# Kernel tuning notes

Measured on AMD Instinct MI355X. Metric: run time of the kernel, lower is better.

The kernel has to match this reference:

```python
import jax, jax.numpy as jnp
import numpy as np

N_ATOMS = 65536
N_PAIRS = N_ATOMS * 32
MAXZ = 95          # D3 tables cover H..Pu, indexed directly by atomic number
NREF = 5           # number of reference coordination numbers per element
CUTOFF, CUTON = 12.0, 10.0   # model units; distances_model2Bohr == 1
K1, K3 = 16.0, -4.0
SMALL = 1e-30      # fp32 stand-in for the original's 1e-300 double guard


def setup_inputs() -> dict:
    key = jax.random.key(0)
    k0, k1, k2, k3 = jax.random.split(key, 4)
    rng = np.random.default_rng(0)

    atomic_numbers = jax.random.randint(k0, (N_ATOMS,), 1, 87)
    idx_i = jax.random.randint(k1, (N_PAIRS,), 0, N_ATOMS)
    idx_j = jax.random.randint(k2, (N_PAIRS,), 0, N_ATOMS)
    # pair distances spanning inside/switch/outside of the 10..12 cutoff band
    distances = jax.random.uniform(k3, (N_PAIRS,), minval=0.8, maxval=12.5)

    # synthetic stand-ins for the grimme_d3 data files
    rcov = jnp.asarray(rng.uniform(0.5, 3.0, (MAXZ,)).astype(np.float32))
    rcn_np = rng.uniform(0.0, 5.0, (MAXZ, NREF)).astype(np.float32)
    rcn_np[::3, NREF - 1] = -1.0  # mimic -1 padding for missing references
    rcn = jnp.asarray(rcn_np)
    rc6 = jnp.asarray(rng.uniform(1.0, 50.0, (MAXZ, MAXZ, NREF, NREF)).astype(np.float32))
    r2r4 = jnp.asarray(rng.uniform(1.0, 10.0, (MAXZ,)).astype(np.float32))

    s6 = jnp.float32(1.0)
    s8 = jnp.float32(0.9171)
    a1 = jnp.float32(0.3385)
    a2 = jnp.float32(2.883)
    return dict(distances=distances, rcov=rcov, rcn=rcn, rc6=rc6, r2r4=r2r4,
                s6=s6, s8=s8, a1=a1, a2=a2,
                atomic_numbers=atomic_numbers, idx_i=idx_i, idx_j=idx_j)


def reference(distances, rcov, rcn, rc6, r2r4, s6, s8, a1, a2,
              atomic_numbers, idx_i, idx_j):
    n = atomic_numbers.shape[0]
    zi = atomic_numbers[idx_i]
    zj = atomic_numbers[idx_j]

    # smooth switch-off from 1 (r < cuton) to 0 (r >= cutoff)
    x = (CUTOFF - distances) / (CUTOFF - CUTON)
    sw = jnp.where(distances < CUTON, 1.0,
                   jnp.where(distances >= CUTOFF, 0.0,
                             ((6.0 * x - 15.0) * x + 10.0) * x * x * x))

    # coordination numbers via inverse damping, scatter-summed per atom i
    rcov_ij = rcov[zi] + rcov[zj]
    cn_ij = sw / (1.0 + jnp.exp(-K1 * (rcov_ij / distances - 1.0)))
    cn = jax.ops.segment_sum(cn_ij, idx_i, num_segments=n)  # [N]

    # Gaussian weights over reference CNs (soft retrieval into rc6 table)
    rcn_a = rcn[atomic_numbers]                 # [N, NREF]
    mask = rcn_a >= 0
    dcn = rcn_a - cn[:, None]
    gw = jnp.where(mask, jnp.exp(K3 * dcn * dcn), 0.0)
    norm = jnp.sum(gw, axis=-1, keepdims=True)
    # exceptional case: all gaussians underflow -> pick the max reference CN
    rcn_max_a = jnp.max(rcn, axis=-1)[atomic_numbers][:, None]
    exceptional = (rcn_a == rcn_max_a).astype(gw.dtype)
    weights = jnp.where(norm == 0, exceptional, gw / jnp.maximum(norm, SMALL))  # [N, NREF]

    # weighted pairwise C6 from reference table rc6[Zi, Zj, a, b]
    w_i = weights[idx_i]                         # [P, NREF]
    w_j = weights[idx_j]                         # [P, NREF]
    c6 = jnp.einsum('pa,pb,pab->p', w_i, w_j, rc6[zi, zj])

    # C8 = 3 * C6 * <r2>/<r4>_i * <r2>/<r4>_j ; BJ critical radius
    qq = 3.0 * r2r4[zi] * r2r4[zj]
    rr = a1 * jnp.sqrt(qq) + a2

    d2 = distances * distances
    d6 = d2 * d2 * d2
    d8 = d6 * d2
    rr2 = rr * rr
    rr6 = rr2 * rr2 * rr2
    rr8 = rr6 * rr2

    # BJ-damped dispersion energy per pair (0.5 for double counting), switched
    e_pair = -0.5 * (s6 * c6 / (d6 + rr6) + s8 * qq * c6 / (d8 + rr8)) * sw

    # per-atom dispersion energies (energies_Hartree2model == 1)
    return jax.ops.segment_sum(e_pair, idx_i, num_segments=n)
```

## Files before the change

### kernel.cpp

```cpp
#include <hip/hip_runtime.h>
#include <stdint.h>


typedef unsigned short u16;
#define MAXZ 95
#define NREF 5
#define EXC_CUT -87.33654f
#define NB    1024
#define BSH   6
#define BSZ   64
#define CAPSH 12
#define SBLOCKS 256
#define TILE  16384
#define RC_TOTAL (MAXZ * MAXZ * 32)

__device__ __forceinline__ float h2f(u16 h) {
    union { _Float16 h; u16 u; } v; v.u = h; return (float)v.h;
}
__device__ __forceinline__ u16 f2h(float f) {
    union { _Float16 h; u16 u; } v; v.h = (_Float16)f; return v.u;
}

__device__ __forceinline__ float switch_fn(float d) {
    if (d < 10.0f) return 1.0f;
    float x = (12.0f - d) * 0.5f;
    return ((6.0f * x - 15.0f) * x + 10.0f) * x * x * x;
}

__device__ __forceinline__ void calc_weights(const float* __restrict__ rcn_z,
                                             float cni, float* __restrict__ w) {
    float r[NREF], arg[NREF];
    float rmax = -1e30f, marg = -1e30f;
#pragma unroll
    for (int a = 0; a < NREF; a++) {
        r[a] = rcn_z[a];
        rmax = fmaxf(rmax, r[a]);
        float dc = r[a] - cni;
        arg[a] = (-4.0f * dc) * dc;
        if (r[a] >= 0.0f) marg = fmaxf(marg, arg[a]);
    }
    if (marg < EXC_CUT) {
#pragma unroll
        for (int a = 0; a < NREF; a++) w[a] = (r[a] == rmax) ? 1.0f : 0.0f;
    } else {
        float g[NREF], norm = 0.0f;
#pragma unroll
        for (int a = 0; a < NREF; a++) {
            float e = (r[a] >= 0.0f) ? expf(arg[a]) : 0.0f;
            g[a] = e;
            norm += e;
        }
        float inv = 1.0f / fmaxf(norm, 1e-30f);
#pragma unroll
        for (int a = 0; a < NREF; a++) w[a] = g[a] * inv;
    }
}

__global__ __launch_bounds__(1024) void scatter_pairs(const float* __restrict__ dist,
                                                      const int* __restrict__ idx_i,
                                                      const int* __restrict__ idx_j,
                                                      const int* __restrict__ Z,
                                                      const float* __restrict__ rcov,
                                                      const float* __restrict__ rc6,
                                                      float* __restrict__ rcovA,
                                                      u16* __restrict__ rc6pad,
                                                      uint32_t* __restrict__ bcount,
                                                      uint2* __restrict__ recs,
                                                      int n_pairs, int n_atoms,
                                                      int chunk) {
    __shared__ uint2 stage[TILE];
    __shared__ uint32_t hist[NB];
    __shared__ uint32_t startb[NB];
    __shared__ uint32_t cur[NB];
    __shared__ uint32_t res[NB];
    __shared__ uint32_t wsum[16];

    int tid = (int)threadIdx.x;
    int g = blockIdx.x * 1024 + tid;
    int T = gridDim.x * 1024;
    for (int i = g; i < n_atoms; i += T) rcovA[i] = rcov[Z[i]];
    for (int id = g; id < RC_TOTAL; id += T) {
        int tile = id >> 5, slot = id & 31;
        rc6pad[id] = (slot < 25) ? f2h(rc6[(size_t)tile * 25 + slot]) : (u16)0;
    }

    int lo = blockIdx.x * chunk;
    int hi = min(lo + chunk, n_pairs);

    for (int t0 = lo; t0 < hi; t0 += TILE) {
        int tend = min(t0 + TILE, hi);
        hist[tid] = 0;
        __syncthreads();

        uint32_t rx[16], ry[16], vm = 0;
#pragma unroll
        for (int it = 0; it < 4; it++) {
            int q0 = t0 + tid * 4 + it * 4096;
            int m = (q0 < tend) ? min(4, tend - q0) : 0;
            float d4[4]; int i4[4], j4[4];
            if (m == 4) {
                float4 dv = *(const float4*)(dist + q0);
                int4 iv = *(const int4*)(idx_i + q0);
                int4 jv = *(const int4*)(idx_j + q0);
                d4[0] = dv.x; d4[1] = dv.y; d4[2] = dv.z; d4[3] = dv.w;
                i4[0] = iv.x; i4[1] = iv.y; i4[2] = iv.z; i4[3] = iv.w;
                j4[0] = jv.x; j4[1] = jv.y; j4[2] = jv.z; j4[3] = jv.w;
            } else {
                for (int s = 0; s < m; s++) {
                    d4[s] = dist[q0 + s]; i4[s] = idx_i[q0 + s]; j4[s] = idx_j[q0 + s];
                }
            }
#pragma unroll
            for (int s = 0; s < 4; s++) {
                int k = it * 4 + s;
                rx[k] = 0u; ry[k] = 0u;
                if (s < m && d4[s] < 12.0f) {
                    uint32_t i = (uint32_t)i4[s];
                    uint32_t b = i >> BSH;
                    rx[k] = __float_as_uint(d4[s]);
                    ry[k] = ((uint32_t)j4[s] & 0xFFFFu) |
                            ((i & (BSZ - 1u)) << 16) | (b << 22);
                    vm |= (1u << k);
                    atomicAdd(&hist[b], 1u);
                }
            }
        }
        __syncthreads();

        {
            uint32_t h = hist[tid];
            int lane = tid & 63, w = tid >> 6;
            uint32_t inc = h;
#pragma unroll
            for (int off = 1; off < 64; off <<= 1) {
                uint32_t v = __shfl_up(inc, off, 64);
                if (lane >= off) inc += v;
            }
            if (lane == 63) wsum[w] = inc;
            __syncthreads();
            if (tid < 16) {
                uint32_t v = wsum[tid];
                uint32_t s = v;
#pragma unroll
                for (int off = 1; off < 16; off <<= 1) {
                    uint32_t u = __shfl_up(s, off, 64);
                    if (tid >= off) s += u;
                }
                wsum[tid] = s - v;
            }
            __syncthreads();
            uint32_t sb = (inc - h) + wsum[w];
            startb[tid] = sb;
            cur[tid] = sb;
            res[tid] = h ? atomicAdd(&bcount[tid], h) : 0u;
        }
        __syncthreads();

#pragma unroll
        for (int k = 0; k < 16; k++) {
            if (vm & (1u << k)) {
                uint32_t b = ry[k] >> 22;
                uint32_t pos = atomicAdd(&cur[b], 1u);
                stage[pos] = make_uint2(rx[k], ry[k]);
            }
        }
        __syncthreads();

        uint32_t total = startb[NB - 1] + hist[NB - 1];
        for (uint32_t t = (uint32_t)tid; t < total; t += 1024u) {
            uint2 r = stage[t];
            uint32_t b = r.y >> 22;
            uint32_t gpos = res[b] + (t - startb[b]);
            if (gpos < (1u << CAPSH))
                recs[((size_t)b << CAPSH) + gpos] =
                    make_uint2(r.x, r.y & 0x3FFFFFu);
        }
        __syncthreads();
    }
}

__global__ __launch_bounds__(256) void cn_weights_bucket(const uint2* __restrict__ recs,
                                                         const uint32_t* __restrict__ bcount,
                                                         const float* __restrict__ rcovA,
                                                         const int* __restrict__ Z,
                                                         const float* __restrict__ rcn,
                                                         const float* __restrict__ r2r4,
                                                         uint4* __restrict__ arec_h,
                                                         int n_atoms) {
    __shared__ float lrc[BSZ];
    __shared__ float acc[BSZ];
    int b = blockIdx.x;
    int base = b << BSH;
    if (threadIdx.x < BSZ) {
        int i = base + (int)threadIdx.x;
        lrc[threadIdx.x] = (i < n_atoms) ? rcovA[i] : 0.0f;
        acc[threadIdx.x] = 0.0f;
    }
    __syncthreads();
    uint32_t n = min(bcount[b], 1u << CAPSH);
    const uint2* r0 = recs + ((size_t)b << CAPSH);
    if (n) {
        uint32_t nm1 = n - 1;
        uint32_t k = threadIdx.x;
        uint2 recA = r0[min(k, nm1)];
        uint2 recB = r0[min(k + 256, nm1)];
        float rjA = rcovA[recA.y & 0xFFFF];
        for (; k < n; k += 256) {
            uint2 recC = r0[min(k + 512, nm1)];
            float rjB = rcovA[recB.y & 0xFFFF];
            float d = __uint_as_float(recA.x);
            int il = (recA.y >> 16) & (BSZ - 1);
            float rij = lrc[il] + rjA;
            float sw = switch_fn(d);
            atomicAdd(&acc[il], sw / (1.0f + expf(-16.0f * (rij / d - 1.0f))));
            recA = recB; recB = recC; rjA = rjB;
        }
    }
    __syncthreads();
    if (threadIdx.x < BSZ) {
        int i = base + (int)threadIdx.x;
        if (i < n_atoms) {
            int z = Z[i];
            float w[NREF];
            calc_weights(rcn + (size_t)z * NREF, acc[threadIdx.x], w);
            uint4 pk;
            pk.x = (uint32_t)f2h(w[0]) | ((uint32_t)f2h(w[1]) << 16);
            pk.y = (uint32_t)f2h(w[2]) | ((uint32_t)f2h(w[3]) << 16);
            pk.z = (uint32_t)f2h(w[4]) | ((uint32_t)f2h(r2r4[z]) << 16);
            pk.w = (uint32_t)z;
            arec_h[i] = pk;
        }
    }
}

__global__ __launch_bounds__(256) void energy_bucket(const uint2* __restrict__ recs,
                                                     const uint32_t* __restrict__ bcount,
                                                     const uint4* __restrict__ arec_h,
                                                     const u16* __restrict__ rc6pad,
                                                     const float* __restrict__ s6p,
                                                     const float* __restrict__ s8p,
                                                     const float* __restrict__ a1p,
                                                     const float* __restrict__ a2p,
                                                     float* __restrict__ eout,
                                                     int n_atoms) {
    __shared__ float4 la0[BSZ];
    __shared__ float4 la1[BSZ];
    __shared__ float  acc[BSZ];
    int b = blockIdx.x;
    int base = b << BSH;
    if (threadIdx.x < BSZ) {
        int i = min(base + (int)threadIdx.x, n_atoms - 1);
        uint4 pk = arec_h[i];
        la0[threadIdx.x] = make_float4(h2f(pk.x & 0xFFFFu), h2f(pk.x >> 16),
                                       h2f(pk.y & 0xFFFFu), h2f(pk.y >> 16));
        la1[threadIdx.x] = make_float4(h2f(pk.z & 0xFFFFu), h2f(pk.z >> 16),
                                       __int_as_float((int)pk.w), 0.0f);
        acc[threadIdx.x] = 0.0f;
    }
    __syncthreads();
    float s6 = s6p[0], s8 = s8p[0], a1 = a1p[0], a2 = a2p[0];
    uint32_t n = min(bcount[b], 1u << CAPSH);
    const uint2* r0 = recs + ((size_t)b << CAPSH);
    if (n) {
        uint32_t nm1 = n - 1;
        uint32_t k = threadIdx.x;
        uint2 recA = r0[min(k, nm1)];
        uint2 recB = r0[min(k + 256, nm1)];
        uint4 pjA = arec_h[recA.y & 0xFFFFu];
        for (; k < n; k += 256) {
            uint2 recC = r0[min(k + 512, nm1)];
            uint4 pjB = arec_h[recB.y & 0xFFFFu];

            int il = (recA.y >> 16) & (BSZ - 1);
            float4 ai1 = la1[il];
            int zi = __float_as_int(ai1.z);
            int zj = (int)pjA.w;
            const uint4* T4 = (const uint4*)(rc6pad + (size_t)(zi * MAXZ + zj) * 32);
            uint4 t0 = T4[0], t1 = T4[1], t2 = T4[2];
            uint32_t t3 = ((const uint32_t*)T4)[12];

            float d = __uint_as_float(recA.x);
            float4 ai0 = la0[il];
            float wi[NREF] = {ai0.x, ai0.y, ai0.z, ai0.w, ai1.x};
            float wj[NREF] = {h2f(pjA.x & 0xFFFFu), h2f(pjA.x >> 16),
                              h2f(pjA.y & 0xFFFFu), h2f(pjA.y >> 16),
                              h2f(pjA.z & 0xFFFFu)};
            float r2r4j = h2f(pjA.z >> 16);

            float tt[25];
            uint32_t tw[12] = {t0.x, t0.y, t0.z, t0.w, t1.x, t1.y, t1.z, t1.w,
                               t2.x, t2.y, t2.z, t2.w};
#pragma unroll
            for (int k2 = 0; k2 < 12; k2++) {
                tt[2 * k2]     = h2f((u16)(tw[k2] & 0xFFFFu));
                tt[2 * k2 + 1] = h2f((u16)(tw[k2] >> 16));
            }
            tt[24] = h2f((u16)(t3 & 0xFFFFu));

            float c6 = 0.0f;
#pragma unroll
            for (int a = 0; a < NREF; a++) {
                float ss = 0.0f;
#pragma unroll
                for (int bb = 0; bb < NREF; bb++) ss = fmaf(wj[bb], tt[a * NREF + bb], ss);
                c6 = fmaf(wi[a], ss, c6);
            }

            float qq = 3.0f * ai1.y * r2r4j;
            float rr = a1 * sqrtf(qq) + a2;
            float d2 = d * d;
            float d6 = d2 * d2 * d2;
            float d8 = d6 * d2;
            float rr2 = rr * rr;
            float rr6 = rr2 * rr2 * rr2;
            float rr8 = rr6 * rr2;
            float sw = switch_fn(d);

            float e = -0.5f * (s6 * c6 / (d6 + rr6) + s8 * qq * c6 / (d8 + rr8)) * sw;
            atomicAdd(&acc[il], e);

            recA = recB; recB = recC; pjA = pjB;
        }
    }
    __syncthreads();
    if (threadIdx.x < BSZ) {
        int i = base + (int)threadIdx.x;
        if (i < n_atoms) eout[i] = acc[threadIdx.x];
    }
}

__global__ __launch_bounds__(256) void pair_cn_slim(const float* __restrict__ dist,
                                                    const float* __restrict__ rcov,
                                                    const int* __restrict__ Z,
                                                    const int* __restrict__ idx_i,
                                                    const int* __restrict__ idx_j,
                                                    float* __restrict__ cn,
                                                    int n_pairs) {
    int p = blockIdx.x * blockDim.x + threadIdx.x;
    if (p >= n_pairs) return;
    float d = dist[p];
    if (d >= 12.0f) return;
    float rij = rcov[Z[idx_i[p]]] + rcov[Z[idx_j[p]]];
    float sw = switch_fn(d);
    atomicAdd(&cn[idx_i[p]], sw / (1.0f + expf(-16.0f * (rij / d - 1.0f))));
}

__global__ __launch_bounds__(256) void pair_energy_slim(const float* __restrict__ dist,
                                                        const int* __restrict__ Z,
                                                        const int* __restrict__ idx_i,
                                                        const int* __restrict__ idx_j,
                                                        const float* __restrict__ cn,
                                                        const float* __restrict__ rcn,
                                                        const float* __restrict__ r2r4,
                                                        const float* __restrict__ rc6,
                                                        const float* __restrict__ s6p,
                                                        const float* __restrict__ s8p,
                                                        const float* __restrict__ a1p,
                                                        const float* __restrict__ a2p,
                                                        float* __restrict__ eout,
                                                        int n_pairs) {
    int p = blockIdx.x * blockDim.x + threadIdx.x;
    if (p >= n_pairs) return;
    float d = dist[p];
    if (d >= 12.0f) return;
    int i = idx_i[p], j = idx_j[p];
    int zi = Z[i], zj = Z[j];
    float wi[NREF], wj[NREF];
    calc_weights(rcn + (size_t)zi * NREF, cn[i], wi);
    calc_weights(rcn + (size_t)zj * NREF, cn[j], wj);
    const float* T = rc6 + (size_t)(zi * MAXZ + zj) * 25;
    float c6 = 0.0f;
#pragma unroll
    for (int a = 0; a < NREF; a++) {
        float s = 0.0f;
#pragma unroll
        for (int bb = 0; bb < NREF; bb++) s = fmaf(wj[bb], T[a * NREF + bb], s);
        c6 = fmaf(wi[a], s, c6);
    }
    float qq = 3.0f * r2r4[zi] * r2r4[zj];
    float rr = a1p[0] * sqrtf(qq) + a2p[0];
    float d2 = d * d;
    float d6 = d2 * d2 * d2;
    float d8 = d6 * d2;
    float rr2 = rr * rr;
    float rr6 = rr2 * rr2 * rr2;
    float rr8 = rr6 * rr2;
    float sw = switch_fn(d);
    float e = -0.5f * (s6p[0] * c6 / (d6 + rr6) + s8p[0] * qq * c6 / (d8 + rr8)) * sw;
    atomicAdd(&eout[i], e);
}

extern "C" void kernel_launch(void* const* d_in, const int* in_sizes, int n_in,
                              void* d_out, int out_size, void* d_ws, size_t ws_size,
                              hipStream_t stream) {
    const float* dist = (const float*)d_in[0];
    const float* rcov = (const float*)d_in[1];
    const float* rcn  = (const float*)d_in[2];
    const float* rc6  = (const float*)d_in[3];
    const float* r2r4 = (const float*)d_in[4];
    const float* s6p  = (const float*)d_in[5];
    const float* s8p  = (const float*)d_in[6];
    const float* a1p  = (const float*)d_in[7];
    const float* a2p  = (const float*)d_in[8];
    const int* Z    = (const int*)d_in[9];
    const int* idxi = (const int*)d_in[10];
    const int* idxj = (const int*)d_in[11];
    float* out = (float*)d_out;

    int n_pairs = in_sizes[0];
    int n_atoms = in_sizes[9];

    char* ws = (char*)d_ws;
    size_t o_bcount = 0;
    size_t o_rcovA  = 4096;
    size_t o_arec   = (o_rcovA + (size_t)n_atoms * 4 + 15) & ~(size_t)15;
    size_t o_rc6    = (o_arec + (size_t)n_atoms * 16 + 63) & ~(size_t)63;
    size_t o_recs   = (o_rc6 + (size_t)RC_TOTAL * 2 + 255) & ~(size_t)255;
    size_t need     = o_recs + ((size_t)NB << CAPSH) * 8;

    uint32_t* bcount = (uint32_t*)(ws + o_bcount);
    float* rcovA  = (float*)(ws + o_rcovA);
    uint4* arec_h = (uint4*)(ws + o_arec);
    u16*   rcpad  = (u16*)(ws + o_rc6);
    uint2* recs   = (uint2*)(ws + o_recs);

    if (ws_size >= need && n_atoms <= NB * BSZ && n_atoms <= 65536) {
        hipMemsetAsync(bcount, 0, NB * 4, stream);
        int chunk = (n_pairs + SBLOCKS - 1) / SBLOCKS;
        scatter_pairs<<<SBLOCKS, 1024, 0, stream>>>(dist, idxi, idxj, Z, rcov, rc6,
                                                    rcovA, rcpad, bcount, recs,
                                                    n_pairs, n_atoms, chunk);
        cn_weights_bucket<<<NB, 256, 0, stream>>>(recs, bcount, rcovA, Z, rcn, r2r4,
                                                  arec_h, n_atoms);
        energy_bucket<<<NB, 256, 0, stream>>>(recs, bcount, arec_h, rcpad,
                                              s6p, s8p, a1p, a2p, out, n_atoms);
    } else {
        int pgrid = (n_pairs + 255) / 256;
        float* cn = (float*)(ws + o_rcovA);
        hipMemsetAsync(out, 0, (size_t)n_atoms * 4, stream);
        hipMemsetAsync(cn, 0, (size_t)n_atoms * 4, stream);
        pair_cn_slim<<<pgrid, 256, 0, stream>>>(dist, rcov, Z, idxi, idxj, cn, n_pairs);
        pair_energy_slim<<<pgrid, 256, 0, stream>>>(dist, Z, idxi, idxj, cn, rcn, r2r4,
                                                    rc6, s6p, s8p, a1p, a2p, out, n_pairs);
    }
}
```

Before: 139.3 us.

## Fuse CN-weights and energy passes into one cooperative kernel with grid sync

Merges the coordination-number/weights kernel and the energy kernel into one cooperative launch, separated by a grid-wide barrier. The goal is to save one kernel launch and its inter-kernel gap. If the cooperative launch fails, it falls back to the two separate kernels. It also halves the number of scatter blocks from 256 to 128. In exchange, the grid sync costs time, and 1024 co-resident blocks of 256 threads are needed, which may limit occupancy or make the cooperative launch fail.

```diff
diff --git a/kernel.cpp b/kernel.cpp
--- a/kernel.cpp
+++ b/kernel.cpp
@@ -1,6 +1,9 @@
 #include <hip/hip_runtime.h>
+#include <hip/hip_cooperative_groups.h>
 #include <stdint.h>
 
+
+namespace cg = cooperative_groups;
 
 typedef unsigned short u16;
 #define MAXZ 95
@@ -10,7 +13,7 @@
 #define BSH   6
 #define BSZ   64
 #define CAPSH 12
-#define SBLOCKS 256
+#define SBLOCKS 128
 #define TILE  16384
 #define RC_TOTAL (MAXZ * MAXZ * 32)
 
@@ -179,16 +182,17 @@
     }
 }
 
-__global__ __launch_bounds__(256) void cn_weights_bucket(const uint2* __restrict__ recs,
-                                                         const uint32_t* __restrict__ bcount,
-                                                         const float* __restrict__ rcovA,
-                                                         const int* __restrict__ Z,
-                                                         const float* __restrict__ rcn,
-                                                         const float* __restrict__ r2r4,
-                                                         uint4* __restrict__ arec_h,
-                                                         int n_atoms) {
-    __shared__ float lrc[BSZ];
-    __shared__ float acc[BSZ];
+
+__device__ __forceinline__ void cn_phase(const uint2* __restrict__ recs,
+                                         const uint32_t* __restrict__ bcount,
+                                         const float* __restrict__ rcovA,
+                                         const int* __restrict__ Z,
+                                         const float* __restrict__ rcn,
+                                         const float* __restrict__ r2r4,
+                                         uint4* __restrict__ arec_h,
+                                         int n_atoms,
+                                         float* __restrict__ lrc,
+                                         float* __restrict__ acc) {
     int b = blockIdx.x;
     int base = b << BSH;
     if (threadIdx.x < BSZ) {
@@ -233,6 +237,140 @@
     }
 }
 
+__device__ __forceinline__ void energy_phase(const uint2* __restrict__ recs,
+                                             const uint32_t* __restrict__ bcount,
+                                             const uint4* __restrict__ arec_h,
+                                             const u16* __restrict__ rc6pad,
+                                             float s6, float s8, float a1, float a2,
+                                             float* __restrict__ eout,
+                                             int n_atoms,
+                                             float4* __restrict__ la0,
+                                             float4* __restrict__ la1,
+                                             float* __restrict__ acc) {
+    int b = blockIdx.x;
+    int base = b << BSH;
+    if (threadIdx.x < BSZ) {
+        int i = min(base + (int)threadIdx.x, n_atoms - 1);
+        uint4 pk = arec_h[i];
+        la0[threadIdx.x] = make_float4(h2f(pk.x & 0xFFFFu), h2f(pk.x >> 16),
+                                       h2f(pk.y & 0xFFFFu), h2f(pk.y >> 16));
+        la1[threadIdx.x] = make_float4(h2f(pk.z & 0xFFFFu), h2f(pk.z >> 16),
+                                       __int_as_float((int)pk.w), 0.0f);
+        acc[threadIdx.x] = 0.0f;
+    }
+    __syncthreads();
+    uint32_t n = min(bcount[b], 1u << CAPSH);
+    const uint2* r0 = recs + ((size_t)b << CAPSH);
+    if (n) {
+        uint32_t nm1 = n - 1;
+        uint32_t k = threadIdx.x;
+        uint2 recA = r0[min(k, nm1)];
+        uint2 recB = r0[min(k + 256, nm1)];
+        uint4 pjA = arec_h[recA.y & 0xFFFFu];
+        for (; k < n; k += 256) {
+            uint2 recC = r0[min(k + 512, nm1)];
+            uint4 pjB = arec_h[recB.y & 0xFFFFu];
+
+            int il = (recA.y >> 16) & (BSZ - 1);
+            float4 ai1 = la1[il];
+            int zi = __float_as_int(ai1.z);
+            int zj = (int)pjA.w;
+            const uint4* T4 = (const uint4*)(rc6pad + (size_t)(zi * MAXZ + zj) * 32);
+            uint4 t0 = T4[0], t1 = T4[1], t2 = T4[2];
+            uint32_t t3 = ((const uint32_t*)T4)[12];
+
+            float d = __uint_as_float(recA.x);
+            float4 ai0 = la0[il];
+            float wi[NREF] = {ai0.x, ai0.y, ai0.z, ai0.w, ai1.x};
+            float wj[NREF] = {h2f(pjA.x & 0xFFFFu), h2f(pjA.x >> 16),
+                              h2f(pjA.y & 0xFFFFu), h2f(pjA.y >> 16),
+                              h2f(pjA.z & 0xFFFFu)};
+            float r2r4j = h2f(pjA.z >> 16);
+
+            float tt[25];
+            uint32_t tw[12] = {t0.x, t0.y, t0.z, t0.w, t1.x, t1.y, t1.z, t1.w,
+                               t2.x, t2.y, t2.z, t2.w};
+#pragma unroll
+            for (int k2 = 0; k2 < 12; k2++) {
+                tt[2 * k2]     = h2f((u16)(tw[k2] & 0xFFFFu));
+                tt[2 * k2 + 1] = h2f((u16)(tw[k2] >> 16));
+            }
+            tt[24] = h2f((u16)(t3 & 0xFFFFu));
+
+            float c6 = 0.0f;
+#pragma unroll
+            for (int a = 0; a < NREF; a++) {
+                float ss = 0.0f;
+#pragma unroll
+                for (int bb = 0; bb < NREF; bb++) ss = fmaf(wj[bb], tt[a * NREF + bb], ss);
+                c6 = fmaf(wi[a], ss, c6);
+            }
+
+            float qq = 3.0f * ai1.y * r2r4j;
+            float rr = a1 * sqrtf(qq) + a2;
+            float d2 = d * d;
+            float d6 = d2 * d2 * d2;
+            float d8 = d6 * d2;
+            float rr2 = rr * rr;
+            float rr6 = rr2 * rr2 * rr2;
+            float rr8 = rr6 * rr2;
+            float sw = switch_fn(d);
+
+            float e = -0.5f * (s6 * c6 / (d6 + rr6) + s8 * qq * c6 / (d8 + rr8)) * sw;
+            atomicAdd(&acc[il], e);
+
+            recA = recB; recB = recC; pjA = pjB;
+        }
+    }
+    __syncthreads();
+    if (threadIdx.x < BSZ) {
+        int i = base + (int)threadIdx.x;
+        if (i < n_atoms) eout[i] = acc[threadIdx.x];
+    }
+}
+
+__global__ __launch_bounds__(256) void cn_energy_fused(const uint2* __restrict__ recs,
+                                                       const uint32_t* __restrict__ bcount,
+                                                       const float* __restrict__ rcovA,
+                                                       const int* __restrict__ Z,
+                                                       const float* __restrict__ rcn,
+                                                       const float* __restrict__ r2r4,
+                                                       uint4* __restrict__ arec_h,
+                                                       const u16* __restrict__ rc6pad,
+                                                       const float* __restrict__ s6p,
+                                                       const float* __restrict__ s8p,
+                                                       const float* __restrict__ a1p,
+                                                       const float* __restrict__ a2p,
+                                                       float* __restrict__ eout,
+                                                       int n_atoms) {
+    __shared__ float lrc[BSZ];
+    __shared__ float accc[BSZ];
+    __shared__ float4 la0[BSZ];
+    __shared__ float4 la1[BSZ];
+    __shared__ float acce[BSZ];
+
+    cn_phase(recs, bcount, rcovA, Z, rcn, r2r4, arec_h, n_atoms, lrc, accc);
+
+    cg::this_grid().sync();
+
+    float s6 = s6p[0], s8 = s8p[0], a1 = a1p[0], a2 = a2p[0];
+    energy_phase(recs, bcount, arec_h, rc6pad, s6, s8, a1, a2, eout, n_atoms,
+                 la0, la1, acce);
+}
+
+__global__ __launch_bounds__(256) void cn_weights_bucket(const uint2* __restrict__ recs,
+                                                         const uint32_t* __restrict__ bcount,
+                                                         const float* __restrict__ rcovA,
+                                                         const int* __restrict__ Z,
+                                                         const float* __restrict__ rcn,
+                                                         const float* __restrict__ r2r4,
+                                                         uint4* __restrict__ arec_h,
+                                                         int n_atoms) {
+    __shared__ float lrc[BSZ];
+    __shared__ float acc[BSZ];
+    cn_phase(recs, bcount, rcovA, Z, rcn, r2r4, arec_h, n_atoms, lrc, acc);
+}
+
 __global__ __launch_bounds__(256) void energy_bucket(const uint2* __restrict__ recs,
                                                      const uint32_t* __restrict__ bcount,
                                                      const uint4* __restrict__ arec_h,
@@ -245,88 +383,10 @@
                                                      int n_atoms) {
     __shared__ float4 la0[BSZ];
     __shared__ float4 la1[BSZ];
-    __shared__ float  acc[BSZ];
-    int b = blockIdx.x;
-    int base = b << BSH;
-    if (threadIdx.x < BSZ) {
-        int i = min(base + (int)threadIdx.x, n_atoms - 1);
-        uint4 pk = arec_h[i];
-        la0[threadIdx.x] = make_float4(h2f(pk.x & 0xFFFFu), h2f(pk.x >> 16),
-                                       h2f(pk.y & 0xFFFFu), h2f(pk.y >> 16));
-        la1[threadIdx.x] = make_float4(h2f(pk.z & 0xFFFFu), h2f(pk.z >> 16),
-                                       __int_as_float((int)pk.w), 0.0f);
-        acc[threadIdx.x] = 0.0f;
-    }
-    __syncthreads();
+    __shared__ float acc[BSZ];
     float s6 = s6p[0], s8 = s8p[0], a1 = a1p[0], a2 = a2p[0];
-    uint32_t n = min(bcount[b], 1u << CAPSH);
-    const uint2* r0 = recs + ((size_t)b << CAPSH);
-    if (n) {
-        uint32_t nm1 = n - 1;
-        uint32_t k = threadIdx.x;
-        uint2 recA = r0[min(k, nm1)];
-        uint2 recB = r0[min(k + 256, nm1)];
-        uint4 pjA = arec_h[recA.y & 0xFFFFu];
-        for (; k < n; k += 256) {
-            uint2 recC = r0[min(k + 512, nm1)];
-            uint4 pjB = arec_h[recB.y & 0xFFFFu];
-
-            int il = (recA.y >> 16) & (BSZ - 1);
-            float4 ai1 = la1[il];
-            int zi = __float_as_int(ai1.z);
-            int zj = (int)pjA.w;
-            const uint4* T4 = (const uint4*)(rc6pad + (size_t)(zi * MAXZ + zj) * 32);
-            uint4 t0 = T4[0], t1 = T4[1], t2 = T4[2];
-            uint32_t t3 = ((const uint32_t*)T4)[12];
-
-            float d = __uint_as_float(recA.x);
-            float4 ai0 = la0[il];
-            float wi[NREF] = {ai0.x, ai0.y, ai0.z, ai0.w, ai1.x};
-            float wj[NREF] = {h2f(pjA.x & 0xFFFFu), h2f(pjA.x >> 16),
-                              h2f(pjA.y & 0xFFFFu), h2f(pjA.y >> 16),
-                              h2f(pjA.z & 0xFFFFu)};
-            float r2r4j = h2f(pjA.z >> 16);
-
-            float tt[25];
-            uint32_t tw[12] = {t0.x, t0.y, t0.z, t0.w, t1.x, t1.y, t1.z, t1.w,
-                               t2.x, t2.y, t2.z, t2.w};
-#pragma unroll
-            for (int k2 = 0; k2 < 12; k2++) {
-                tt[2 * k2]     = h2f((u16)(tw[k2] & 0xFFFFu));
-                tt[2 * k2 + 1] = h2f((u16)(tw[k2] >> 16));
-            }
-            tt[24] = h2f((u16)(t3 & 0xFFFFu));
-
-            float c6 = 0.0f;
-#pragma unroll
-            for (int a = 0; a < NREF; a++) {
-                float ss = 0.0f;
-#pragma unroll
-                for (int bb = 0; bb < NREF; bb++) ss = fmaf(wj[bb], tt[a * NREF + bb], ss);
-                c6 = fmaf(wi[a], ss, c6);
-            }
-
-            float qq = 3.0f * ai1.y * r2r4j;
-            float rr = a1 * sqrtf(qq) + a2;
-            float d2 = d * d;
-            float d6 = d2 * d2 * d2;
-            float d8 = d6 * d2;
-            float rr2 = rr * rr;
-            float rr6 = rr2 * rr2 * rr2;
-            float rr8 = rr6 * rr2;
-            float sw = switch_fn(d);
-
-            float e = -0.5f * (s6 * c6 / (d6 + rr6) + s8 * qq * c6 / (d8 + rr8)) * sw;
-            atomicAdd(&acc[il], e);
-
-            recA = recB; recB = recC; pjA = pjB;
-        }
-    }
-    __syncthreads();
-    if (threadIdx.x < BSZ) {
-        int i = base + (int)threadIdx.x;
-        if (i < n_atoms) eout[i] = acc[threadIdx.x];
-    }
+    energy_phase(recs, bcount, arec_h, rc6pad, s6, s8, a1, a2, eout, n_atoms,
+                 la0, la1, acc);
 }
 
 __global__ __launch_bounds__(256) void pair_cn_slim(const float* __restrict__ dist,
@@ -430,10 +490,39 @@
         scatter_pairs<<<SBLOCKS, 1024, 0, stream>>>(dist, idxi, idxj, Z, rcov, rc6,
                                                     rcovA, rcpad, bcount, recs,
                                                     n_pairs, n_atoms, chunk);
-        cn_weights_bucket<<<NB, 256, 0, stream>>>(recs, bcount, rcovA, Z, rcn, r2r4,
-                                                  arec_h, n_atoms);
-        energy_bucket<<<NB, 256, 0, stream>>>(recs, bcount, arec_h, rcpad,
-                                              s6p, s8p, a1p, a2p, out, n_atoms);
+
+        static int coop_ok = -1;
+        if (coop_ok < 0) {
+            int dev = 0, v = 0;
+            hipGetDevice(&dev);
+            hipDeviceGetAttribute(&v, hipDeviceAttributeCooperativeLaunch, dev);
+            coop_ok = v ? 1 : 0;
+        }
+        bool fused = false;
+        if (coop_ok) {
+            const uint2* a_recs = recs; const uint32_t* a_bc = bcount;
+            const float* a_rcovA = rcovA; const int* a_Z = Z;
+            const float* a_rcn = rcn; const float* a_r2r4 = r2r4;
+            uint4* a_arec = arec_h; const u16* a_rcpad = rcpad;
+            const float* a_s6 = s6p; const float* a_s8 = s8p;
+            const float* a_a1 = a1p; const float* a_a2 = a2p;
+            float* a_out = out; int a_na = n_atoms;
+            void* args[] = {(void*)&a_recs, (void*)&a_bc, (void*)&a_rcovA,
+                            (void*)&a_Z, (void*)&a_rcn, (void*)&a_r2r4,
+                            (void*)&a_arec, (void*)&a_rcpad, (void*)&a_s6,
+                            (void*)&a_s8, (void*)&a_a1, (void*)&a_a2,
+                            (void*)&a_out, (void*)&a_na};
+            hipError_t e = hipLaunchCooperativeKernel((const void*)cn_energy_fused,
+                                                      dim3(NB), dim3(256), args,
+                                                      0, stream);
+            if (e == hipSuccess) fused = true; else coop_ok = 0;
+        }
+        if (!fused) {
+            cn_weights_bucket<<<NB, 256, 0, stream>>>(recs, bcount, rcovA, Z, rcn,
+                                                      r2r4, arec_h, n_atoms);
+            energy_bucket<<<NB, 256, 0, stream>>>(recs, bcount, arec_h, rcpad,
+                                                  s6p, s8p, a1p, a2p, out, n_atoms);
+        }
     } else {
         int pgrid = (n_pairs + 255) / 256;
         float* cn = (float*)(ws + o_rcovA);
```

Result: slower. 260.4 us (+86.9%).
